# Performance work log

Measured on AMD Instinct MI355X. Metric: run time of the kernel, lower is better.

Reference implementation:

```python
import jax, jax.numpy as jnp
import numpy as np

N = 8192
IN_F = 128
OUT_F = 64
ALPHA = 0.2  # LeakyReLU negative slope
NEG_BIG = -9e15

def _xavier(key, shape, gain=1.414):
    fan_in, fan_out = shape[0], shape[1]
    limit = gain * np.sqrt(6.0 / (fan_in + fan_out))
    return jax.random.uniform(key, shape, jnp.float32, -limit, limit)

def setup_inputs() -> dict:
    key = jax.random.key(0)
    k1, k2, k3, k4 = jax.random.split(key, 4)
    h = jax.random.normal(k1, (N, IN_F), jnp.float32)
    adj = jax.random.randint(k2, (N, N), 0, 2, jnp.int32)
    W = _xavier(k3, (IN_F, OUT_F))
    a = _xavier(k4, (2 * OUT_F, 1))
    return {"h": h, "adj": adj, "W": W, "a": a}

def reference(h, adj, W, a):
    Wh = h @ W                                  # [N, OUT_F]
    a1 = a[:OUT_F, 0]                           # [OUT_F]
    a2 = a[OUT_F:, 0]                           # [OUT_F]
    e = (Wh @ a1)[:, None] + (Wh @ a2)[None, :] # [N, N] additive score
    e = jnp.where(e > 0, e, ALPHA * e)          # LeakyReLU
    e = jnp.where(adj > 0, e, NEG_BIG)          # mask non-edges
    attention = jax.nn.softmax(e, axis=1)       # [N, N]
    h_prime = attention @ Wh                    # [N, OUT_F]
    return jax.nn.elu(h_prime)                  # concat=True path
```

## Files before the change

### kernel.cpp

```cpp
#include <hip/hip_runtime.h>
#include <hip/hip_bf16.h>
#include <math.h>

#define NN 8192
#define INF_ 128
#define OUTF 64

typedef __attribute__((ext_vector_type(4))) float f32x4;
typedef __attribute__((ext_vector_type(2))) int i32x2;
typedef __attribute__((ext_vector_type(8))) unsigned short u16x8;
typedef __attribute__((ext_vector_type(8))) __bf16 bf16x8;

#define BAR()                                                    \
    {                                                            \
        asm volatile("s_waitcnt lgkmcnt(0)" ::: "memory");       \
        __builtin_amdgcn_s_barrier();                            \
    }

__device__ __forceinline__ unsigned short f2bf(float f) {
    unsigned int u = __float_as_uint(f);
    u = (u + 0x7FFFu + ((u >> 16) & 1u)) >> 16;
    return (unsigned short)u;
}

__global__ __launch_bounds__(256) void prep_kernel(
    const float* __restrict__ h, const float* __restrict__ W,
    const float* __restrict__ a, unsigned short* __restrict__ WhT,
    float* __restrict__ f1, float* __restrict__ f2)
{
    __shared__ float W_lds[INF_ * OUTF];
    __shared__ float h_lds[32 * INF_];
    __shared__ unsigned short t_lds[OUTF * 34];

    const int t = threadIdx.x;
    const int rb = blockIdx.x * 32;

    {
        const float4* Ws = (const float4*)W;
        float4* Wd = (float4*)W_lds;
        #pragma unroll
        for (int q = 0; q < 8; ++q) Wd[t + 256 * q] = Ws[t + 256 * q];
        const float4* hs = (const float4*)(h + (size_t)rb * INF_);
        float4* hd = (float4*)h_lds;
        #pragma unroll
        for (int q = 0; q < 4; ++q) hd[t + 256 * q] = hs[t + 256 * q];
    }
    __syncthreads();

    const int lane = t & 63;
    const int w = t >> 6;

    float acc[8];
    #pragma unroll
    for (int q = 0; q < 8; ++q) acc[q] = 0.f;
    for (int k = 0; k < INF_; ++k) {
        const float wv = W_lds[k * OUTF + lane];
        #pragma unroll
        for (int q = 0; q < 8; ++q)
            acc[q] = fmaf(h_lds[(w * 8 + q) * INF_ + k], wv, acc[q]);
    }

    const float a1 = a[lane];
    const float a2 = a[OUTF + lane];
    #pragma unroll
    for (int q = 0; q < 8; ++q) {
        float s1 = acc[q] * a1;
        float s2 = acc[q] * a2;
        #pragma unroll
        for (int m = 1; m < 64; m <<= 1) {
            s1 += __shfl_xor(s1, m, 64);
            s2 += __shfl_xor(s2, m, 64);
        }
        if (lane == 0) {
            f1[rb + w * 8 + q] = s1;
            f2[rb + w * 8 + q] = s2;
        }
        t_lds[lane * 34 + w * 8 + q] = f2bf(acc[q]);
    }
    __syncthreads();
    {
        const int c = t >> 2;
        const int ro = (t & 3) * 8;
        unsigned int pk[4];
        #pragma unroll
        for (int i = 0; i < 4; ++i) {
            const unsigned int lo = t_lds[c * 34 + ro + 2 * i];
            const unsigned int hi = t_lds[c * 34 + ro + 2 * i + 1];
            pk[i] = lo | (hi << 16);
        }
        *(uint4*)(WhT + (size_t)c * NN + rb + ro) = make_uint4(pk[0], pk[1], pk[2], pk[3]);
    }
}

__global__ __launch_bounds__(1024) void fmax_kernel(
    const float* __restrict__ f2, float* __restrict__ f2max)
{
    __shared__ float red[16];
    const int t = threadIdx.x;
    float m = -INFINITY;
    #pragma unroll
    for (int q = 0; q < NN / 1024; ++q) m = fmaxf(m, f2[t + q * 1024]);
    #pragma unroll
    for (int s = 1; s < 64; s <<= 1) m = fmaxf(m, __shfl_xor(m, s, 64));
    if ((t & 63) == 0) red[t >> 6] = m;
    __syncthreads();
    if (t == 0) {
        float r = red[0];
        #pragma unroll
        for (int i = 1; i < 16; ++i) r = fmaxf(r, red[i]);
        f2max[0] = r;
    }
}

__global__ __launch_bounds__(256) void repack_kernel(
    const unsigned short* __restrict__ WhT, unsigned short* __restrict__ WhTs)
{
    const int ch = blockIdx.x;
    const int t = threadIdx.x;
    const int qd = t >> 6, l = t & 63;
    const int r = l & 15, g = l >> 4;
    const u16x8 v = *(const u16x8*)(WhT + (size_t)(qd * 16 + r) * NN + ch * 32 + g * 8);
    *(u16x8*)(WhTs + (size_t)ch * 2048 + qd * 512 + l * 8) = v;
}

__global__ __launch_bounds__(1024) void bd_kernel(
    const float* __restrict__ f2, unsigned int* __restrict__ bd)
{
    const int i = blockIdx.x * 1024 + threadIdx.x;
    const float v = f2[i];
    const unsigned int B = f2bf(expf(v));
    const unsigned int D = f2bf(expf(0.2f * v));
    bd[i] = B | (D << 16);
}

__global__ __launch_bounds__(512) void gatz_kernel(
    const int* __restrict__ adj, const unsigned short* __restrict__ WhTs,
    const float* __restrict__ f1, const unsigned int* __restrict__ bd,
    const float* __restrict__ f2max, float* __restrict__ out)
{
    __shared__ float acc_lds[8 * 16 * OUTF];
    __shared__ unsigned int bd_lds[NN];
    __shared__ float l_lds[8 * 16];

    const int t = threadIdx.x;
    const int lane = t & 63;
    const int w = t >> 6;
    const int r = lane & 15;
    const int g = lane >> 4;
    const int row_base = blockIdx.x * 16;

    #pragma unroll
    for (int q = 0; q < 4; ++q)
        ((uint4*)bd_lds)[t + 512 * q] = ((const uint4*)bd)[t + 512 * q];

    const float f1r = f1[row_base + r];
    float Mr = f1r + f2max[0];
    Mr = fmaxf(Mr, 0.2f * Mr);
    const float A = expf(f1r - Mr);
    const float C = expf(0.2f * f1r - Mr);
    const unsigned int THb = (unsigned int)f2bf(expf(-f1r));

    f32x4 accl = {0.f, 0.f, 0.f, 0.f};
    f32x4 acc[4];
    #pragma unroll
    for (int q = 0; q < 4; ++q) acc[q] = accl;

    u16x8 ones_u;
    #pragma unroll
    for (int i = 0; i < 8; ++i) ones_u[i] = 0x3F80;
    const bf16x8 bones = __builtin_bit_cast(bf16x8, ones_u);

    const int j0 = w * 1024;
    const int* base = adj + (size_t)row_base * NN + j0 + 2 * lane;
    const u16x8* wv = (const u16x8*)WhTs + lane;

    i32x2 st[16];
    #pragma unroll
    for (int rr = 0; rr < 16; ++rr)
        st[rr] = *(const i32x2*)(base + (size_t)rr * NN);

    BAR();

    for (int s = 0; s < 8; ++s) {
        unsigned long long k0 = 0ull, k1 = 0ull;
        #pragma unroll
        for (int rr = 0; rr < 16; ++rr) {
            const i32x2 v = st[rr];
            const unsigned long long b0 = __ballot(v[0] > 0);
            const unsigned long long b1 = __ballot(v[1] > 0);
            if (rr == r) { k0 = b0; k1 = b1; }
        }
        if (s + 1 < 8) {
            #pragma unroll
            for (int rr = 0; rr < 16; ++rr)
                st[rr] = *(const i32x2*)(base + (size_t)rr * NN + (s + 1) * 128);
        }
        #pragma unroll
        for (int cc = 0; cc < 4; ++cc) {
            const int jl = s * 128 + cc * 32;
            const int col = j0 + jl + g * 8;
            const int ch = (j0 + jl) >> 5;
            const unsigned int sh = 16 * cc + 4 * g;
            const unsigned int m0 = (unsigned int)(k0 >> sh) & 0xFu;
            const unsigned int m1 = (unsigned int)(k1 >> sh) & 0xFu;
            const uint4 bq0 = *(const uint4*)(bd_lds + col);
            const uint4 bq1 = *(const uint4*)(bd_lds + col + 4);
            const unsigned int bdv[8] = {bq0.x, bq0.y, bq0.z, bq0.w,
                                         bq1.x, bq1.y, bq1.z, bq1.w};

            u16x8 pb;
            #pragma unroll
            for (int i = 0; i < 8; ++i) {
                const unsigned int v = bdv[i];
                const unsigned int bb = v & 0xFFFFu;
                const bool up = bb > THb;
                const unsigned int sel = up ? bb : (v >> 16);
                const float f = __uint_as_float(sel << 16);
                const float as = up ? A : C;
                const unsigned int bit = (((i & 1) ? m1 : m0) >> (i >> 1)) & 1u;
                const float p = bit ? f * as : 0.f;
                pb[i] = __builtin_bit_cast(unsigned short, __float2bfloat16(p));
            }

            const bf16x8 af = __builtin_bit_cast(bf16x8, pb);
            #pragma unroll
            for (int qd = 0; qd < 4; ++qd) {
                const bf16x8 bq = __builtin_bit_cast(bf16x8, wv[((size_t)ch * 4 + qd) * 64]);
                acc[qd] = __builtin_amdgcn_mfma_f32_16x16x32_bf16(af, bq, acc[qd], 0, 0, 0);
            }
            accl = __builtin_amdgcn_mfma_f32_16x16x32_bf16(af, bones, accl, 0, 0, 0);
        }
    }

    if (r == 0) {
        #pragma unroll
        for (int q = 0; q < 4; ++q) l_lds[w * 16 + 4 * g + q] = accl[q];
    }
    #pragma unroll
    for (int q = 0; q < 4; ++q) {
        const int m = 4 * g + q;
        #pragma unroll
        for (int qd = 0; qd < 4; ++qd)
            acc_lds[(w * 16 + m) * OUTF + qd * 16 + r] = acc[qd][q];
    }
    __syncthreads();

    {
        #pragma unroll
        for (int hh = 0; hh < 2; ++hh) {
            const int idx = t + hh * 512;
            const int row = idx >> 6;
            const int col = idx & 63;
            float L = 0.f, o = 0.f;
            #pragma unroll
            for (int ww = 0; ww < 8; ++ww) {
                L += l_lds[ww * 16 + row];
                o += acc_lds[(ww * 16 + row) * OUTF + col];
            }
            o /= L;
            o = (o > 0.f) ? o : expm1f(o);
            out[(size_t)(row_base + row) * OUTF + col] = o;
        }
    }
}

extern "C" void kernel_launch(void* const* d_in, const int* in_sizes, int n_in,
                              void* d_out, int out_size, void* d_ws, size_t ws_size,
                              hipStream_t stream) {
    const float* h = (const float*)d_in[0];
    const int* adj = (const int*)d_in[1];
    const float* W = (const float*)d_in[2];
    const float* a = (const float*)d_in[3];
    float* out = (float*)d_out;

    char* ws = (char*)d_ws;
    unsigned short* WhT = (unsigned short*)ws;
    unsigned short* WhTs = (unsigned short*)(ws + (1 << 20));
    float* f1 = (float*)(ws + (2 << 20));
    float* f2 = f1 + NN;
    float* f2m = f2 + NN;
    unsigned int* bd = (unsigned int*)(f2m + 64);

    prep_kernel<<<NN / 32, 256, 0, stream>>>(h, W, a, WhT, f1, f2);
    fmax_kernel<<<1, 1024, 0, stream>>>(f2, f2m);
    bd_kernel<<<NN / 1024, 1024, 0, stream>>>(f2, bd);
    repack_kernel<<<NN / 32, 256, 0, stream>>>(WhT, WhTs);
    gatz_kernel<<<NN / 16, 512, 0, stream>>>(adj, WhTs, f1, bd, f2m, out);
}
```

Measured before the change: 76.77 us.

## Split adjacency bitmask build into separate phase staged through LDS

The main attention kernel now first streams each wave's two full adjacency rows with coalesced 16-byte loads, converts them to ballot bitmasks stored in LDS, then runs the MFMA accumulation phase reading masks from LDS. The exp-table (bd) is no longer copied into LDS and is read directly from global/cache. This separates the memory-bound adjacency read from compute to get wider, more sequential loads, at the cost of losing overlap between adj loading and MFMA work and adding a barrier plus global reads of bd in the inner loop.

```diff
diff --git a/kernel.cpp b/kernel.cpp
--- a/kernel.cpp
+++ b/kernel.cpp
@@ -7,15 +7,9 @@
 #define OUTF 64
 
 typedef __attribute__((ext_vector_type(4))) float f32x4;
-typedef __attribute__((ext_vector_type(2))) int i32x2;
+typedef __attribute__((ext_vector_type(4))) int i32x4;
 typedef __attribute__((ext_vector_type(8))) unsigned short u16x8;
 typedef __attribute__((ext_vector_type(8))) __bf16 bf16x8;
-
-#define BAR()                                                    \
-    {                                                            \
-        asm volatile("s_waitcnt lgkmcnt(0)" ::: "memory");       \
-        __builtin_amdgcn_s_barrier();                            \
-    }
 
 __device__ __forceinline__ unsigned short f2bf(float f) {
     unsigned int u = __float_as_uint(f);
@@ -133,13 +127,15 @@
     bd[i] = B | (D << 16);
 }
 
-__global__ __launch_bounds__(512) void gatz_kernel(
+#define MQW 129
+
+__global__ __launch_bounds__(512) void gatp_kernel(
     const int* __restrict__ adj, const unsigned short* __restrict__ WhTs,
     const float* __restrict__ f1, const unsigned int* __restrict__ bd,
     const float* __restrict__ f2max, float* __restrict__ out)
 {
+    __shared__ unsigned long long mask_lds[16 * MQW];
     __shared__ float acc_lds[8 * 16 * OUTF];
-    __shared__ unsigned int bd_lds[NN];
     __shared__ float l_lds[8 * 16];
 
     const int t = threadIdx.x;
@@ -149,9 +145,30 @@
     const int g = lane >> 4;
     const int row_base = blockIdx.x * 16;
 
-    #pragma unroll
-    for (int q = 0; q < 4; ++q)
-        ((uint4*)bd_lds)[t + 512 * q] = ((const uint4*)bd)[t + 512 * q];
+    {
+        const i32x4* src = (const i32x4*)(adj + (size_t)row_base * NN + w * 16384);
+        i32x4 st[8];
+        #pragma unroll
+        for (int k = 0; k < 8; ++k) st[k] = src[k * 64 + lane];
+
+        for (int it = 0; it < 64; ++it) {
+            const i32x4 v = st[it & 7];
+            if (it + 8 < 64) st[it & 7] = src[(it + 8) * 64 + lane];
+            unsigned long long b0 = __ballot(v[0] > 0);
+            unsigned long long b1 = __ballot(v[1] > 0);
+            unsigned long long b2 = __ballot(v[2] > 0);
+            unsigned long long b3 = __ballot(v[3] > 0);
+            const int rr = 2 * w + (it >> 5);
+            const int q = it & 31;
+            if (lane < 4) {
+                unsigned long long x = b0;
+                x = (lane == 1) ? b1 : x;
+                x = (lane == 2) ? b2 : x;
+                x = (lane == 3) ? b3 : x;
+                mask_lds[rr * MQW + q * 4 + lane] = x;
+            }
+        }
+    }
 
     const float f1r = f1[row_base + r];
     float Mr = f1r + f2max[0];
@@ -170,65 +187,54 @@
     for (int i = 0; i < 8; ++i) ones_u[i] = 0x3F80;
     const bf16x8 bones = __builtin_bit_cast(bf16x8, ones_u);
 
-    const int j0 = w * 1024;
-    const int* base = adj + (size_t)row_base * NN + j0 + 2 * lane;
-    const u16x8* wv = (const u16x8*)WhTs + lane;
-
-    i32x2 st[16];
-    #pragma unroll
-    for (int rr = 0; rr < 16; ++rr)
-        st[rr] = *(const i32x2*)(base + (size_t)rr * NN);
-
-    BAR();
-
-    for (int s = 0; s < 8; ++s) {
-        unsigned long long k0 = 0ull, k1 = 0ull;
-        #pragma unroll
-        for (int rr = 0; rr < 16; ++rr) {
-            const i32x2 v = st[rr];
-            const unsigned long long b0 = __ballot(v[0] > 0);
-            const unsigned long long b1 = __ballot(v[1] > 0);
-            if (rr == r) { k0 = b0; k1 = b1; }
-        }
-        if (s + 1 < 8) {
+    __syncthreads();
+
+    {
+        const u16x8* wv = (const u16x8*)WhTs + lane;
+        #pragma unroll
+        for (int qq = 0; qq < 4; ++qq) {
+            const int qg = w * 4 + qq;
+            const unsigned long long mq0 = mask_lds[r * MQW + qg * 4 + 0];
+            const unsigned long long mq1 = mask_lds[r * MQW + qg * 4 + 1];
+            const unsigned long long mq2 = mask_lds[r * MQW + qg * 4 + 2];
+            const unsigned long long mq3 = mask_lds[r * MQW + qg * 4 + 3];
             #pragma unroll
-            for (int rr = 0; rr < 16; ++rr)
-                st[rr] = *(const i32x2*)(base + (size_t)rr * NN + (s + 1) * 128);
-        }
-        #pragma unroll
-        for (int cc = 0; cc < 4; ++cc) {
-            const int jl = s * 128 + cc * 32;
-            const int col = j0 + jl + g * 8;
-            const int ch = (j0 + jl) >> 5;
-            const unsigned int sh = 16 * cc + 4 * g;
-            const unsigned int m0 = (unsigned int)(k0 >> sh) & 0xFu;
-            const unsigned int m1 = (unsigned int)(k1 >> sh) & 0xFu;
-            const uint4 bq0 = *(const uint4*)(bd_lds + col);
-            const uint4 bq1 = *(const uint4*)(bd_lds + col + 4);
-            const unsigned int bdv[8] = {bq0.x, bq0.y, bq0.z, bq0.w,
-                                         bq1.x, bq1.y, bq1.z, bq1.w};
-
-            u16x8 pb;
-            #pragma unroll
-            for (int i = 0; i < 8; ++i) {
-                const unsigned int v = bdv[i];
-                const unsigned int bb = v & 0xFFFFu;
-                const bool up = bb > THb;
-                const unsigned int sel = up ? bb : (v >> 16);
-                const float f = __uint_as_float(sel << 16);
-                const float as = up ? A : C;
-                const unsigned int bit = (((i & 1) ? m1 : m0) >> (i >> 1)) & 1u;
-                const float p = bit ? f * as : 0.f;
-                pb[i] = __builtin_bit_cast(unsigned short, __float2bfloat16(p));
+            for (int cq = 0; cq < 8; ++cq) {
+                const int ch = qg * 8 + cq;
+                const int col = ch * 32 + g * 8;
+                const unsigned int shq = 8 * cq + 2 * g;
+                const unsigned int e0 = (unsigned int)(mq0 >> shq) & 3u;
+                const unsigned int e1 = (unsigned int)(mq1 >> shq) & 3u;
+                const unsigned int e2 = (unsigned int)(mq2 >> shq) & 3u;
+                const unsigned int e3 = (unsigned int)(mq3 >> shq) & 3u;
+                const uint4 bq0 = *(const uint4*)(bd + col);
+                const uint4 bq1 = *(const uint4*)(bd + col + 4);
+                const unsigned int bdv[8] = {bq0.x, bq0.y, bq0.z, bq0.w,
+                                             bq1.x, bq1.y, bq1.z, bq1.w};
+                const unsigned int eb[4] = {e0, e1, e2, e3};
+
+                u16x8 pb;
+                #pragma unroll
+                for (int i = 0; i < 8; ++i) {
+                    const unsigned int v = bdv[i];
+                    const unsigned int bb = v & 0xFFFFu;
+                    const bool up = bb > THb;
+                    const unsigned int sel = up ? bb : (v >> 16);
+                    const float f = __uint_as_float(sel << 16);
+                    const float as = up ? A : C;
+                    const unsigned int bit = (eb[i & 3] >> (i >> 2)) & 1u;
+                    const float p = bit ? f * as : 0.f;
+                    pb[i] = __builtin_bit_cast(unsigned short, __float2bfloat16(p));
+                }
+
+                const bf16x8 af = __builtin_bit_cast(bf16x8, pb);
+                #pragma unroll
+                for (int qd = 0; qd < 4; ++qd) {
+                    const bf16x8 bq = __builtin_bit_cast(bf16x8, wv[((size_t)ch * 4 + qd) * 64]);
+                    acc[qd] = __builtin_amdgcn_mfma_f32_16x16x32_bf16(af, bq, acc[qd], 0, 0, 0);
+                }
+                accl = __builtin_amdgcn_mfma_f32_16x16x32_bf16(af, bones, accl, 0, 0, 0);
             }
-
-            const bf16x8 af = __builtin_bit_cast(bf16x8, pb);
-            #pragma unroll
-            for (int qd = 0; qd < 4; ++qd) {
-                const bf16x8 bq = __builtin_bit_cast(bf16x8, wv[((size_t)ch * 4 + qd) * 64]);
-                acc[qd] = __builtin_amdgcn_mfma_f32_16x16x32_bf16(af, bq, acc[qd], 0, 0, 0);
-            }
-            accl = __builtin_amdgcn_mfma_f32_16x16x32_bf16(af, bones, accl, 0, 0, 0);
         }
     }
 
@@ -285,5 +291,5 @@
     fmax_kernel<<<1, 1024, 0, stream>>>(f2, f2m);
     bd_kernel<<<NN / 1024, 1024, 0, stream>>>(f2, bd);
     repack_kernel<<<NN / 32, 256, 0, stream>>>(WhT, WhTs);
-    gatz_kernel<<<NN / 16, 512, 0, stream>>>(adj, WhTs, f1, bd, f2m, out);
-}
+    gatp_kernel<<<NN / 16, 512, 0, stream>>>(adj, WhTs, f1, bd, f2m, out);
+}
```

Result: slower. 104.0 us (+35.5%).

## Split softmax weights into two branch accumulators, drop max-reduction kernel

Applied to the files above, without the earlier changes.

Drops the global max reduction and the per-row max shift. Each LeakyReLU branch now feeds its own MFMA accumulator: raw bf16 exp(f2) or exp(0.2 f2) values are selected by the mask and threshold. The two accumulators are combined at the end with a per-row factor exp(-0.8 f1), which removes the per-element float multiply and bf16 conversion from the inner loop. This doubles the MFMA count and loses max-stabilization, so it depends on exponent ranges staying finite. The adjacency prefetch also moves after the compute, with a sched_barrier.

```diff
diff --git a/kernel.cpp b/kernel.cpp
--- a/kernel.cpp
+++ b/kernel.cpp
@@ -89,26 +89,6 @@
             pk[i] = lo | (hi << 16);
         }
         *(uint4*)(WhT + (size_t)c * NN + rb + ro) = make_uint4(pk[0], pk[1], pk[2], pk[3]);
-    }
-}
-
-__global__ __launch_bounds__(1024) void fmax_kernel(
-    const float* __restrict__ f2, float* __restrict__ f2max)
-{
-    __shared__ float red[16];
-    const int t = threadIdx.x;
-    float m = -INFINITY;
-    #pragma unroll
-    for (int q = 0; q < NN / 1024; ++q) m = fmaxf(m, f2[t + q * 1024]);
-    #pragma unroll
-    for (int s = 1; s < 64; s <<= 1) m = fmaxf(m, __shfl_xor(m, s, 64));
-    if ((t & 63) == 0) red[t >> 6] = m;
-    __syncthreads();
-    if (t == 0) {
-        float r = red[0];
-        #pragma unroll
-        for (int i = 1; i < 16; ++i) r = fmaxf(r, red[i]);
-        f2max[0] = r;
     }
 }
 
@@ -136,7 +116,7 @@
 __global__ __launch_bounds__(512) void gatz_kernel(
     const int* __restrict__ adj, const unsigned short* __restrict__ WhTs,
     const float* __restrict__ f1, const unsigned int* __restrict__ bd,
-    const float* __restrict__ f2max, float* __restrict__ out)
+    float* __restrict__ out)
 {
     __shared__ float acc_lds[8 * 16 * OUTF];
     __shared__ unsigned int bd_lds[NN];
@@ -154,16 +134,18 @@
         ((uint4*)bd_lds)[t + 512 * q] = ((const uint4*)bd)[t + 512 * q];
 
     const float f1r = f1[row_base + r];
-    float Mr = f1r + f2max[0];
-    Mr = fmaxf(Mr, 0.2f * Mr);
-    const float A = expf(f1r - Mr);
-    const float C = expf(0.2f * f1r - Mr);
     const unsigned int THb = (unsigned int)f2bf(expf(-f1r));
 
-    f32x4 accl = {0.f, 0.f, 0.f, 0.f};
-    f32x4 acc[4];
-    #pragma unroll
-    for (int q = 0; q < 4; ++q) acc[q] = accl;
+    float Ev[4];
+    #pragma unroll
+    for (int q = 0; q < 4; ++q)
+        Ev[q] = expf(-0.8f * f1[row_base + 4 * g + q]);
+
+    f32x4 alB = {0.f, 0.f, 0.f, 0.f};
+    f32x4 alD = alB;
+    f32x4 accB[4], accD[4];
+    #pragma unroll
+    for (int q = 0; q < 4; ++q) { accB[q] = alB; accD[q] = alB; }
 
     u16x8 ones_u;
     #pragma unroll
@@ -190,58 +172,69 @@
             const unsigned long long b1 = __ballot(v[1] > 0);
             if (rr == r) { k0 = b0; k1 = b1; }
         }
-        if (s + 1 < 8) {
-            #pragma unroll
-            for (int rr = 0; rr < 16; ++rr)
-                st[rr] = *(const i32x2*)(base + (size_t)rr * NN + (s + 1) * 128);
-        }
+
         #pragma unroll
         for (int cc = 0; cc < 4; ++cc) {
-            const int jl = s * 128 + cc * 32;
-            const int col = j0 + jl + g * 8;
-            const int ch = (j0 + jl) >> 5;
+            const int ch = w * 32 + s * 4 + cc;
+            const int col = ch * 32 + g * 8;
             const unsigned int sh = 16 * cc + 4 * g;
             const unsigned int m0 = (unsigned int)(k0 >> sh) & 0xFu;
             const unsigned int m1 = (unsigned int)(k1 >> sh) & 0xFu;
+
+            u16x8 wq[4];
+            #pragma unroll
+            for (int qd = 0; qd < 4; ++qd)
+                wq[qd] = wv[((size_t)ch * 4 + qd) * 64];
+
             const uint4 bq0 = *(const uint4*)(bd_lds + col);
             const uint4 bq1 = *(const uint4*)(bd_lds + col + 4);
             const unsigned int bdv[8] = {bq0.x, bq0.y, bq0.z, bq0.w,
                                          bq1.x, bq1.y, bq1.z, bq1.w};
 
-            u16x8 pb;
+            u16x8 pbB, pbD;
             #pragma unroll
             for (int i = 0; i < 8; ++i) {
                 const unsigned int v = bdv[i];
                 const unsigned int bb = v & 0xFFFFu;
+                const unsigned int bit = (((i & 1) ? m1 : m0) >> (i >> 1)) & 1u;
                 const bool up = bb > THb;
-                const unsigned int sel = up ? bb : (v >> 16);
-                const float f = __uint_as_float(sel << 16);
-                const float as = up ? A : C;
-                const unsigned int bit = (((i & 1) ? m1 : m0) >> (i >> 1)) & 1u;
-                const float p = bit ? f * as : 0.f;
-                pb[i] = __builtin_bit_cast(unsigned short, __float2bfloat16(p));
+                pbB[i] = (bit && up)  ? (unsigned short)bb        : (unsigned short)0;
+                pbD[i] = (bit && !up) ? (unsigned short)(v >> 16) : (unsigned short)0;
             }
 
-            const bf16x8 af = __builtin_bit_cast(bf16x8, pb);
+            const bf16x8 afB = __builtin_bit_cast(bf16x8, pbB);
+            const bf16x8 afD = __builtin_bit_cast(bf16x8, pbD);
             #pragma unroll
             for (int qd = 0; qd < 4; ++qd) {
-                const bf16x8 bq = __builtin_bit_cast(bf16x8, wv[((size_t)ch * 4 + qd) * 64]);
-                acc[qd] = __builtin_amdgcn_mfma_f32_16x16x32_bf16(af, bq, acc[qd], 0, 0, 0);
+                const bf16x8 bq = __builtin_bit_cast(bf16x8, wq[qd]);
+                accB[qd] = __builtin_amdgcn_mfma_f32_16x16x32_bf16(afB, bq, accB[qd], 0, 0, 0);
+                accD[qd] = __builtin_amdgcn_mfma_f32_16x16x32_bf16(afD, bq, accD[qd], 0, 0, 0);
             }
-            accl = __builtin_amdgcn_mfma_f32_16x16x32_bf16(af, bones, accl, 0, 0, 0);
+            alB = __builtin_amdgcn_mfma_f32_16x16x32_bf16(afB, bones, alB, 0, 0, 0);
+            alD = __builtin_amdgcn_mfma_f32_16x16x32_bf16(afD, bones, alD, 0, 0, 0);
+        }
+
+        __builtin_amdgcn_sched_barrier(0x38F);
+
+        if (s + 1 < 8) {
+            #pragma unroll
+            for (int rr = 0; rr < 16; ++rr)
+                st[rr] = *(const i32x2*)(base + (size_t)rr * NN + (s + 1) * 128);
         }
     }
 
     if (r == 0) {
         #pragma unroll
-        for (int q = 0; q < 4; ++q) l_lds[w * 16 + 4 * g + q] = accl[q];
+        for (int q = 0; q < 4; ++q)
+            l_lds[w * 16 + 4 * g + q] = alB[q] + Ev[q] * alD[q];
     }
     #pragma unroll
     for (int q = 0; q < 4; ++q) {
         const int m = 4 * g + q;
         #pragma unroll
         for (int qd = 0; qd < 4; ++qd)
-            acc_lds[(w * 16 + m) * OUTF + qd * 16 + r] = acc[qd][q];
+            acc_lds[(w * 16 + m) * OUTF + qd * 16 + r] =
+                accB[qd][q] + Ev[q] * accD[qd][q];
     }
     __syncthreads();
 
@@ -278,12 +271,10 @@
     unsigned short* WhTs = (unsigned short*)(ws + (1 << 20));
     float* f1 = (float*)(ws + (2 << 20));
     float* f2 = f1 + NN;
-    float* f2m = f2 + NN;
-    unsigned int* bd = (unsigned int*)(f2m + 64);
+    unsigned int* bd = (unsigned int*)(f2 + NN);
 
     prep_kernel<<<NN / 32, 256, 0, stream>>>(h, W, a, WhT, f1, f2);
-    fmax_kernel<<<1, 1024, 0, stream>>>(f2, f2m);
     bd_kernel<<<NN / 1024, 1024, 0, stream>>>(f2, bd);
     repack_kernel<<<NN / 32, 256, 0, stream>>>(WhT, WhTs);
-    gatz_kernel<<<NN / 16, 512, 0, stream>>>(adj, WhTs, f1, bd, f2m, out);
-}
+    gatz_kernel<<<NN / 16, 512, 0, stream>>>(adj, WhTs, f1, bd, out);
+}
```

Measured after the change: 79.55 us. 1.04x slower.

## Prebuild all adjacency bitmasks upfront with 16-byte loads and double-buffer Wh fragments

Applied to the files above, without the earlier changes.

The adjacency tile is now read entirely before the compute loop. Each lane issues 16-byte loads and builds all ballot masks into registers, so adjacency loading no longer interleaves with the MFMA loop. The compute loop is fully unrolled over 32 chunks, and the WhT fragments are prefetched one chunk ahead into a register double buffer. This aims to cut global-load latency stalls inside the MFMA loop, at the cost of more live registers (the 16 masks plus the double buffer) and a larger unrolled code body.

```diff
diff --git a/kernel.cpp b/kernel.cpp
--- a/kernel.cpp
+++ b/kernel.cpp
@@ -7,7 +7,7 @@
 #define OUTF 64
 
 typedef __attribute__((ext_vector_type(4))) float f32x4;
-typedef __attribute__((ext_vector_type(2))) int i32x2;
+typedef __attribute__((ext_vector_type(4))) int i32x4;
 typedef __attribute__((ext_vector_type(8))) unsigned short u16x8;
 typedef __attribute__((ext_vector_type(8))) __bf16 bf16x8;
 
@@ -133,7 +133,7 @@
     bd[i] = B | (D << 16);
 }
 
-__global__ __launch_bounds__(512) void gatz_kernel(
+__global__ __launch_bounds__(512) void gatw_kernel(
     const int* __restrict__ adj, const unsigned short* __restrict__ WhTs,
     const float* __restrict__ f1, const unsigned int* __restrict__ bd,
     const float* __restrict__ f2max, float* __restrict__ out)
@@ -153,6 +153,36 @@
     for (int q = 0; q < 4; ++q)
         ((uint4*)bd_lds)[t + 512 * q] = ((const uint4*)bd)[t + 512 * q];
 
+    const int j0 = w * 1024;
+    const int* base = adj + (size_t)row_base * NN + j0 + 4 * lane;
+    unsigned long long km[4][4];
+    {
+        i32x4 st[16];
+        #pragma unroll
+        for (int rr = 0; rr < 16; ++rr)
+            st[rr] = *(const i32x4*)(base + (size_t)rr * NN);
+
+        #pragma unroll
+        for (int q = 0; q < 4; ++q) {
+            #pragma unroll
+            for (int rr = 0; rr < 16; ++rr) {
+                const i32x4 v = st[rr];
+                const unsigned long long b0 = __ballot(v[0] > 0);
+                const unsigned long long b1 = __ballot(v[1] > 0);
+                const unsigned long long b2 = __ballot(v[2] > 0);
+                const unsigned long long b3 = __ballot(v[3] > 0);
+                if (rr == r) {
+                    km[q][0] = b0; km[q][1] = b1; km[q][2] = b2; km[q][3] = b3;
+                }
+            }
+            if (q + 1 < 4) {
+                #pragma unroll
+                for (int rr = 0; rr < 16; ++rr)
+                    st[rr] = *(const i32x4*)(base + (size_t)rr * NN + (q + 1) * 256);
+            }
+        }
+    }
+
     const float f1r = f1[row_base + r];
     float Mr = f1r + f2max[0];
     Mr = fmaxf(Mr, 0.2f * Mr);
@@ -170,39 +200,36 @@
     for (int i = 0; i < 8; ++i) ones_u[i] = 0x3F80;
     const bf16x8 bones = __builtin_bit_cast(bf16x8, ones_u);
 
-    const int j0 = w * 1024;
-    const int* base = adj + (size_t)row_base * NN + j0 + 2 * lane;
-    const u16x8* wv = (const u16x8*)WhTs + lane;
-
-    i32x2 st[16];
-    #pragma unroll
-    for (int rr = 0; rr < 16; ++rr)
-        st[rr] = *(const i32x2*)(base + (size_t)rr * NN);
-
     BAR();
 
-    for (int s = 0; s < 8; ++s) {
-        unsigned long long k0 = 0ull, k1 = 0ull;
-        #pragma unroll
-        for (int rr = 0; rr < 16; ++rr) {
-            const i32x2 v = st[rr];
-            const unsigned long long b0 = __ballot(v[0] > 0);
-            const unsigned long long b1 = __ballot(v[1] > 0);
-            if (rr == r) { k0 = b0; k1 = b1; }
-        }
-        if (s + 1 < 8) {
-            #pragma unroll
-            for (int rr = 0; rr < 16; ++rr)
-                st[rr] = *(const i32x2*)(base + (size_t)rr * NN + (s + 1) * 128);
-        }
-        #pragma unroll
-        for (int cc = 0; cc < 4; ++cc) {
-            const int jl = s * 128 + cc * 32;
-            const int col = j0 + jl + g * 8;
-            const int ch = (j0 + jl) >> 5;
-            const unsigned int sh = 16 * cc + 4 * g;
-            const unsigned int m0 = (unsigned int)(k0 >> sh) & 0xFu;
-            const unsigned int m1 = (unsigned int)(k1 >> sh) & 0xFu;
+    {
+        const u16x8* wv = (const u16x8*)WhTs + lane;
+        const int chb = w * 32;
+
+        u16x8 wq0[4], wq1[4];
+        #pragma unroll
+        for (int qd = 0; qd < 4; ++qd)
+            wq0[qd] = wv[((size_t)chb * 4 + qd) * 64];
+
+        #pragma unroll
+        for (int ci = 0; ci < 32; ++ci) {
+            u16x8* cur = (ci & 1) ? wq1 : wq0;
+            u16x8* nxt = (ci & 1) ? wq0 : wq1;
+            if (ci + 1 < 32) {
+                #pragma unroll
+                for (int qd = 0; qd < 4; ++qd)
+                    nxt[qd] = wv[((size_t)(chb + ci + 1) * 4 + qd) * 64];
+            }
+            const int q = ci >> 3, cq = ci & 7;
+            const int ch = chb + ci;
+            const int col = ch * 32 + g * 8;
+            const unsigned int shq = 8 * cq + 2 * g;
+            const unsigned int e0 = (unsigned int)(km[q][0] >> shq) & 3u;
+            const unsigned int e1 = (unsigned int)(km[q][1] >> shq) & 3u;
+            const unsigned int e2 = (unsigned int)(km[q][2] >> shq) & 3u;
+            const unsigned int e3 = (unsigned int)(km[q][3] >> shq) & 3u;
+            const unsigned int eb[4] = {e0, e1, e2, e3};
+
             const uint4 bq0 = *(const uint4*)(bd_lds + col);
             const uint4 bq1 = *(const uint4*)(bd_lds + col + 4);
             const unsigned int bdv[8] = {bq0.x, bq0.y, bq0.z, bq0.w,
@@ -217,7 +244,7 @@
                 const unsigned int sel = up ? bb : (v >> 16);
                 const float f = __uint_as_float(sel << 16);
                 const float as = up ? A : C;
-                const unsigned int bit = (((i & 1) ? m1 : m0) >> (i >> 1)) & 1u;
+                const unsigned int bit = (eb[i & 3] >> (i >> 2)) & 1u;
                 const float p = bit ? f * as : 0.f;
                 pb[i] = __builtin_bit_cast(unsigned short, __float2bfloat16(p));
             }
@@ -225,7 +252,7 @@
             const bf16x8 af = __builtin_bit_cast(bf16x8, pb);
             #pragma unroll
             for (int qd = 0; qd < 4; ++qd) {
-                const bf16x8 bq = __builtin_bit_cast(bf16x8, wv[((size_t)ch * 4 + qd) * 64]);
+                const bf16x8 bq = __builtin_bit_cast(bf16x8, cur[qd]);
                 acc[qd] = __builtin_amdgcn_mfma_f32_16x16x32_bf16(af, bq, acc[qd], 0, 0, 0);
             }
             accl = __builtin_amdgcn_mfma_f32_16x16x32_bf16(af, bones, accl, 0, 0, 0);
@@ -285,5 +312,5 @@
     fmax_kernel<<<1, 1024, 0, stream>>>(f2, f2m);
     bd_kernel<<<NN / 1024, 1024, 0, stream>>>(f2, bd);
     repack_kernel<<<NN / 32, 256, 0, stream>>>(WhT, WhTs);
-    gatz_kernel<<<NN / 16, 512, 0, stream>>>(adj, WhTs, f1, bd, f2m, out);
-}
+    gatw_kernel<<<NN / 16, 512, 0, stream>>>(adj, WhTs, f1, bd, f2m, out);
+}
```

Result: slower. 89.25 us (+16.2%).
